# Optimization experiments

Hardware: AMD Instinct MI355X
Metric: run time of the kernel (lower is better)

The kernel has to match this reference:

```python
import jax, jax.numpy as jnp
import numpy as np

B, H, C_LEN, Q_LEN = 64, 128, 1024, 128


def setup_inputs() -> dict:
    key = jax.random.key(0)
    k1, k2, k3 = jax.random.split(key, 3)
    context = jax.random.normal(k1, (B, H, C_LEN), dtype=jnp.float32)
    question = jax.random.normal(k2, (B, H, Q_LEN), dtype=jnp.float32)
    lim = np.sqrt(1.0 / H)
    w = jax.random.uniform(k3, (3 * H,), dtype=jnp.float32, minval=-lim, maxval=lim)
    return {"context": context, "question": question, "w": w}


def reference(context, question, w):
    # context: (B, H, C), question: (B, H, Q); w: (3H,) with cat order (q, c, cq)
    h = w.shape[0] // 3
    w_q, w_c, w_cq = w[:h], w[h:2 * h], w[2 * h:]
    c = jnp.transpose(context, (0, 2, 1))   # (B, C, H)
    q = jnp.transpose(question, (0, 2, 1))  # (B, Q, H)
    # trilinear similarity s[b,i,j] = c_i.w_c + q_j.w_q + (c_i*w_cq).q_j  -> (B, C, Q)
    s = (c @ w_c)[:, :, None] + (q @ w_q)[:, None, :] \
        + jnp.einsum('bih,bjh->bij', c * w_cq, q)
    # original applies softmax over dim=1 (context axis) for BOTH s1 and s2
    s1 = jax.nn.softmax(s, axis=1)           # (B, C, Q)
    a = jnp.einsum('bij,bjh->bih', s1, q)    # (B, C, H)
    l = jnp.einsum('bij,bkj->bik', s1, s1)   # (B, C, C)
    b = jnp.einsum('bik,bkh->bih', l, c)     # (B, C, H)
    out = jnp.concatenate([c, a, c * a, c * b], axis=2)  # (B, C, 4H)
    # dropout disabled (drop_prob=0) for deterministic reference
    return jnp.transpose(out, (0, 2, 1))     # (B, 4H, C)
```

## Files before the change

### kernel.cpp

```cpp
#include <hip/hip_runtime.h>

#define BB 64
#define HH 128
#define CC 1024
#define QQ 128

typedef unsigned short u16;
typedef unsigned int u32;

__device__ __forceinline__ float lo2f(u32 u) {
  union { float f; u32 i; } v; v.i = u << 16; return v.f;
}
__device__ __forceinline__ float hi2f(u32 u) {
  union { float f; u32 i; } v; v.i = u & 0xFFFF0000u; return v.f;
}
__device__ __forceinline__ u16 f2b(float f) {
  union { float f; u32 i; } v; v.f = f;
  u32 r = v.i + 0x7FFFu + ((v.i >> 16) & 1u);
  return (u16)(r >> 16);
}

__global__ __launch_bounds__(512) void k1_s_softmax(
    const float* __restrict__ ctx, const float* __restrict__ qst,
    const float* __restrict__ w, u16* __restrict__ s1) {
  const int b = blockIdx.y;
  const int j0 = blockIdx.x * 16;
  const int tid = threadIdx.x;
  const float* cb = ctx + (size_t)b * HH * CC;
  const float* qb = qst + (size_t)b * HH * QQ;

  float dotv[16][2];
  float qwq[16];
  float cwc[2] = {0.f, 0.f};
#pragma unroll
  for (int jj = 0; jj < 16; ++jj) {
    qwq[jj] = 0.f;
    dotv[jj][0] = dotv[jj][1] = 0.f;
  }

  for (int h = 0; h < HH; ++h) {
    const float2 cv = *(const float2*)(cb + (size_t)h * CC + tid * 2);
    float c0 = cv.x, c1 = cv.y;
    float wqv = w[h], wcv = w[HH + h], wcqv = w[2 * HH + h];
    cwc[0] += c0 * wcv; cwc[1] += c1 * wcv;
    float t0 = c0 * wcqv, t1 = c1 * wcqv;
    const float4* qrow = (const float4*)(qb + (size_t)h * QQ + j0);
    float4 q0 = qrow[0], q1 = qrow[1], q2 = qrow[2], q3 = qrow[3];
    float qv[16] = {q0.x, q0.y, q0.z, q0.w, q1.x, q1.y, q1.z, q1.w,
                    q2.x, q2.y, q2.z, q2.w, q3.x, q3.y, q3.z, q3.w};
#pragma unroll
    for (int jj = 0; jj < 16; ++jj) {
      qwq[jj] += qv[jj] * wqv;
      dotv[jj][0] += t0 * qv[jj];
      dotv[jj][1] += t1 * qv[jj];
    }
  }
#pragma unroll
  for (int jj = 0; jj < 16; ++jj) {
    float base = qwq[jj];
    dotv[jj][0] += cwc[0] + base;
    dotv[jj][1] += cwc[1] + base;
  }

  __shared__ float red[16 * 512];
  __shared__ float red2[16 * 32];
  __shared__ float bc[16];
  const int rj = tid >> 5, rs = tid & 31;

#pragma unroll
  for (int jj = 0; jj < 16; ++jj)
    red[jj * 512 + tid] = fmaxf(dotv[jj][0], dotv[jj][1]);
  __syncthreads();
  {
    float m = red[rj * 512 + rs * 16];
#pragma unroll
    for (int g = 1; g < 16; ++g) m = fmaxf(m, red[rj * 512 + rs * 16 + g]);
    red2[rj * 32 + rs] = m;
  }
  __syncthreads();
  if (tid < 16) {
    float m = red2[tid * 32];
#pragma unroll
    for (int g = 1; g < 32; ++g) m = fmaxf(m, red2[tid * 32 + g]);
    bc[tid] = m;
  }
  __syncthreads();

#pragma unroll
  for (int jj = 0; jj < 16; ++jj) {
    float mj = bc[jj];
    float e0 = __expf(dotv[jj][0] - mj);
    float e1 = __expf(dotv[jj][1] - mj);
    dotv[jj][0] = e0; dotv[jj][1] = e1;
    red[jj * 512 + tid] = e0 + e1;
  }
  __syncthreads();
  {
    float s = 0.f;
#pragma unroll
    for (int g = 0; g < 16; ++g) s += red[rj * 512 + rs * 16 + g];
    red2[rj * 32 + rs] = s;
  }
  __syncthreads();
  if (tid < 16) {
    float s = 0.f;
#pragma unroll
    for (int g = 0; g < 32; ++g) s += red2[tid * 32 + g];
    bc[tid] = 1.0f / s;
  }
  __syncthreads();

  u16* srow = s1 + ((size_t)b * QQ + j0) * CC + tid * 2;
#pragma unroll
  for (int jj = 0; jj < 16; ++jj) {
    float inv = bc[jj];
    u32 pk = (u32)f2b(dotv[jj][0] * inv) | ((u32)f2b(dotv[jj][1] * inv) << 16);
    *(u32*)(srow + (size_t)jj * CC) = pk;
  }
}

__global__ __launch_bounds__(256) void k2_t(
    const float* __restrict__ ctx, const u16* __restrict__ s1,
    float* __restrict__ t) {
  const int b = blockIdx.y;
  const int tz = blockIdx.x;
  const int tile = tz & 3;
  const int z = tz >> 2;
  const int j0 = (tile & 1) * 64;
  const int h0 = (tile >> 1) * 64;
  const int tid = threadIdx.x;
  const int tj = tid >> 4, th = tid & 15;
  __shared__ float sA[64 * 33];
  __shared__ float sB[64 * 33];
  float acc[4][4];
#pragma unroll
  for (int jj = 0; jj < 4; ++jj)
#pragma unroll
    for (int hh = 0; hh < 4; ++hh) acc[jj][hh] = 0.f;

  const int r = tid >> 2;
  const int sg = (tid & 3) * 8;
  const u16* sbase = s1 + ((size_t)b * QQ + j0 + r) * CC + sg;
  const float* cbase = ctx + ((size_t)b * HH + h0 + r) * CC + sg;

  const int ib0 = z * 256;
  for (int ib = ib0; ib < ib0 + 256; ib += 32) {
    __syncthreads();
    {
      uint4 sv = *(const uint4*)(sbase + ib);
      float* a = &sA[r * 33 + sg];
      a[0] = lo2f(sv.x); a[1] = hi2f(sv.x);
      a[2] = lo2f(sv.y); a[3] = hi2f(sv.y);
      a[4] = lo2f(sv.z); a[5] = hi2f(sv.z);
      a[6] = lo2f(sv.w); a[7] = hi2f(sv.w);
      float4 c0 = *(const float4*)(cbase + ib);
      float4 c1 = *(const float4*)(cbase + ib + 4);
      float* bptr = &sB[r * 33 + sg];
      bptr[0] = c0.x; bptr[1] = c0.y; bptr[2] = c0.z; bptr[3] = c0.w;
      bptr[4] = c1.x; bptr[5] = c1.y; bptr[6] = c1.z; bptr[7] = c1.w;
    }
    __syncthreads();
#pragma unroll 4
    for (int ii = 0; ii < 32; ++ii) {
      float av[4], bv[4];
#pragma unroll
      for (int jj = 0; jj < 4; ++jj) av[jj] = sA[(tj + 16 * jj) * 33 + ii];
#pragma unroll
      for (int hh = 0; hh < 4; ++hh) bv[hh] = sB[(th + 16 * hh) * 33 + ii];
#pragma unroll
      for (int jj = 0; jj < 4; ++jj)
#pragma unroll
        for (int hh = 0; hh < 4; ++hh) acc[jj][hh] += av[jj] * bv[hh];
    }
  }
  float* tp = t + (size_t)b * QQ * HH;
#pragma unroll
  for (int jj = 0; jj < 4; ++jj)
#pragma unroll
    for (int hh = 0; hh < 4; ++hh)
      atomicAdd(&tp[(size_t)(j0 + tj + 16 * jj) * HH + (h0 + th + 16 * hh)],
                acc[jj][hh]);
}

__global__ __launch_bounds__(256) void k3_out(
    const float* __restrict__ ctx, const float* __restrict__ qst,
    const u16* __restrict__ s1, const float* __restrict__ t,
    float* __restrict__ out) {
  const int b = blockIdx.y;
  const int i0 = (blockIdx.x >> 1) * 64;
  const int h0 = (blockIdx.x & 1) * 64;
  const int tid = threadIdx.x;
  const int ti = tid & 15;
  const int th2 = tid >> 4;

  __shared__ float sA[32][65];
  __shared__ float sQ[32][65];
  __shared__ float sT[32][65];

  float accA[4][4], accB[4][4];
#pragma unroll
  for (int ii = 0; ii < 4; ++ii)
#pragma unroll
    for (int hh = 0; hh < 4; ++hh) { accA[ii][hh] = 0.f; accB[ii][hh] = 0.f; }

  for (int jc = 0; jc < QQ; jc += 32) {
    __syncthreads();
    {
      int rr = tid >> 3, col = (tid & 7) * 8;
      uint4 v = *(const uint4*)(s1 + ((size_t)b * QQ + jc + rr) * CC + i0 + col);
      float* dst = &sA[rr][col];
      dst[0] = lo2f(v.x); dst[1] = hi2f(v.x);
      dst[2] = lo2f(v.y); dst[3] = hi2f(v.y);
      dst[4] = lo2f(v.z); dst[5] = hi2f(v.z);
      dst[6] = lo2f(v.w); dst[7] = hi2f(v.w);
    }
    {
      int rr = tid >> 3, col = (tid & 7) * 8;
      const float* p = t + ((size_t)b * QQ + jc + rr) * HH + h0 + col;
      float4 v0 = *(const float4*)p;
      float4 v1 = *(const float4*)(p + 4);
      float* dst = &sT[rr][col];
      dst[0] = v0.x; dst[1] = v0.y; dst[2] = v0.z; dst[3] = v0.w;
      dst[4] = v1.x; dst[5] = v1.y; dst[6] = v1.z; dst[7] = v1.w;
    }
    {
      int hh = tid >> 2, jo = (tid & 3) * 8;
      const float* p = qst + ((size_t)b * HH + h0 + hh) * QQ + jc + jo;
      float4 v0 = *(const float4*)p;
      float4 v1 = *(const float4*)(p + 4);
      sQ[jo + 0][hh] = v0.x; sQ[jo + 1][hh] = v0.y;
      sQ[jo + 2][hh] = v0.z; sQ[jo + 3][hh] = v0.w;
      sQ[jo + 4][hh] = v1.x; sQ[jo + 5][hh] = v1.y;
      sQ[jo + 6][hh] = v1.z; sQ[jo + 7][hh] = v1.w;
    }
    __syncthreads();

#pragma unroll 8
    for (int kk = 0; kk < 32; ++kk) {
      float4 avv = *(const float4*)&sA[kk][ti * 4];
      float4 qvv = *(const float4*)&sQ[kk][th2 * 4];
      float4 tvv = *(const float4*)&sT[kk][th2 * 4];
      float av[4] = {avv.x, avv.y, avv.z, avv.w};
      float qv[4] = {qvv.x, qvv.y, qvv.z, qvv.w};
      float tv[4] = {tvv.x, tvv.y, tvv.z, tvv.w};
#pragma unroll
      for (int ii = 0; ii < 4; ++ii)
#pragma unroll
        for (int hh = 0; hh < 4; ++hh) {
          accA[ii][hh] += av[ii] * qv[hh];
          accB[ii][hh] += av[ii] * tv[hh];
        }
    }
  }

#pragma unroll
  for (int hh = 0; hh < 4; ++hh) {
    int h = h0 + th2 * 4 + hh;
    float4 cv = *(const float4*)(ctx + ((size_t)b * HH + h) * CC + i0 + ti * 4);
    float4 oA = {accA[0][hh], accA[1][hh], accA[2][hh], accA[3][hh]};
    float4 oB = {accB[0][hh], accB[1][hh], accB[2][hh], accB[3][hh]};
    float4 cA = {cv.x * oA.x, cv.y * oA.y, cv.z * oA.z, cv.w * oA.w};
    float4 cB = {cv.x * oB.x, cv.y * oB.y, cv.z * oB.z, cv.w * oB.w};
    size_t ob = (size_t)b * 4 * HH * CC + i0 + ti * 4;
    *(float4*)(out + ob + (size_t)h * CC) = cv;
    *(float4*)(out + ob + (size_t)(HH + h) * CC) = oA;
    *(float4*)(out + ob + (size_t)(2 * HH + h) * CC) = cA;
    *(float4*)(out + ob + (size_t)(3 * HH + h) * CC) = cB;
  }
}

extern "C" void kernel_launch(void* const* d_in, const int* in_sizes, int n_in,
                              void* d_out, int out_size, void* d_ws, size_t ws_size,
                              hipStream_t stream) {
  const float* ctx = (const float*)d_in[0];
  const float* qst = (const float*)d_in[1];
  const float* w = (const float*)d_in[2];
  for (int k = 0; k < n_in; ++k) {
    if (in_sizes[k] == BB * HH * CC) ctx = (const float*)d_in[k];
    else if (in_sizes[k] == BB * HH * QQ) qst = (const float*)d_in[k];
    else if (in_sizes[k] == 3 * HH) w = (const float*)d_in[k];
  }
  float* out = (float*)d_out;

  u16* s1 = (u16*)d_ws;
  float* t = (float*)((char*)d_ws + (size_t)BB * QQ * CC * sizeof(u16));

  k1_s_softmax<<<dim3(QQ / 16, BB), 512, 0, stream>>>(ctx, qst, w, s1);
  hipMemsetAsync(t, 0, (size_t)BB * QQ * HH * sizeof(float), stream);
  k2_t<<<dim3(16, BB), 256, 0, stream>>>(ctx, s1, t);
  k3_out<<<dim3(32, BB), 256, 0, stream>>>(ctx, qst, s1, t, out);
}
```

Before: 304.1 us.

## Port k2/k3 matmuls to bf16 MFMA with hi/lo split and transposed s1 layout

```diff
diff --git a/kernel.cpp b/kernel.cpp
--- a/kernel.cpp
+++ b/kernel.cpp
@@ -7,6 +7,10 @@
 
 typedef unsigned short u16;
 typedef unsigned int u32;
+using bf16x8 = __attribute__((ext_vector_type(8))) short;
+using f32x4 = __attribute__((ext_vector_type(4))) float;
+
+#define MFMA16(a, b, c) __builtin_amdgcn_mfma_f32_16x16x32_bf16(a, b, c, 0, 0, 0)
 
 __device__ __forceinline__ float lo2f(u32 u) {
   union { float f; u32 i; } v; v.i = u << 16; return v.f;
@@ -19,12 +23,41 @@
   u32 r = v.i + 0x7FFFu + ((v.i >> 16) & 1u);
   return (u16)(r >> 16);
 }
+__device__ __forceinline__ u32 pack_hi2(float a, float b) {
+  return (__float_as_uint(a) >> 16) | (__float_as_uint(b) & 0xFFFF0000u);
+}
+__device__ __forceinline__ u32 pack_lo2(float a, float b) {
+  float ra = a - __uint_as_float(__float_as_uint(a) & 0xFFFF0000u);
+  float rb = b - __uint_as_float(__float_as_uint(b) & 0xFFFF0000u);
+  return (__float_as_uint(ra) >> 16) | (__float_as_uint(rb) & 0xFFFF0000u);
+}
+
+__device__ __forceinline__ void stage16(const float* __restrict__ p,
+                                        u16* dhi, u16* dlo) {
+  float4 a0 = *(const float4*)p;
+  float4 a1 = *(const float4*)(p + 4);
+  float4 a2 = *(const float4*)(p + 8);
+  float4 a3 = *(const float4*)(p + 12);
+  uint4 h0 = {pack_hi2(a0.x, a0.y), pack_hi2(a0.z, a0.w),
+              pack_hi2(a1.x, a1.y), pack_hi2(a1.z, a1.w)};
+  uint4 h1 = {pack_hi2(a2.x, a2.y), pack_hi2(a2.z, a2.w),
+              pack_hi2(a3.x, a3.y), pack_hi2(a3.z, a3.w)};
+  uint4 l0 = {pack_lo2(a0.x, a0.y), pack_lo2(a0.z, a0.w),
+              pack_lo2(a1.x, a1.y), pack_lo2(a1.z, a1.w)};
+  uint4 l1 = {pack_lo2(a2.x, a2.y), pack_lo2(a2.z, a2.w),
+              pack_lo2(a3.x, a3.y), pack_lo2(a3.z, a3.w)};
+  *(uint4*)dhi = h0;
+  *(uint4*)(dhi + 8) = h1;
+  *(uint4*)dlo = l0;
+  *(uint4*)(dlo + 8) = l1;
+}
 
 __global__ __launch_bounds__(512) void k1_s_softmax(
     const float* __restrict__ ctx, const float* __restrict__ qst,
-    const float* __restrict__ w, u16* __restrict__ s1) {
-  const int b = blockIdx.y;
-  const int j0 = blockIdx.x * 16;
+    const float* __restrict__ w, u16* __restrict__ s1ws,
+    u16* __restrict__ s1tb) {
+  const int b = blockIdx.x;
+  const int j0 = blockIdx.y * 16;
   const int tid = threadIdx.x;
   const float* cb = ctx + (size_t)b * HH * CC;
   const float* qb = qst + (size_t)b * HH * QQ;
@@ -110,163 +143,181 @@
   }
   __syncthreads();
 
-  u16* srow = s1 + ((size_t)b * QQ + j0) * CC + tid * 2;
 #pragma unroll
   for (int jj = 0; jj < 16; ++jj) {
     float inv = bc[jj];
-    u32 pk = (u32)f2b(dotv[jj][0] * inv) | ((u32)f2b(dotv[jj][1] * inv) << 16);
+    dotv[jj][0] *= inv;
+    dotv[jj][1] *= inv;
+  }
+  u16* srow = s1ws + ((size_t)b * QQ + j0) * CC + tid * 2;
+#pragma unroll
+  for (int jj = 0; jj < 16; ++jj) {
+    u32 pk = (u32)f2b(dotv[jj][0]) | ((u32)f2b(dotv[jj][1]) << 16);
     *(u32*)(srow + (size_t)jj * CC) = pk;
   }
-}
-
-__global__ __launch_bounds__(256) void k2_t(
-    const float* __restrict__ ctx, const u16* __restrict__ s1,
-    float* __restrict__ t) {
-  const int b = blockIdx.y;
-  const int tz = blockIdx.x;
-  const int tile = tz & 3;
-  const int z = tz >> 2;
-  const int j0 = (tile & 1) * 64;
-  const int h0 = (tile >> 1) * 64;
+  u16* stb = s1tb + (size_t)b * (16 * 1024 * 8);
+  const int jg0 = j0 >> 3;
+#pragma unroll
+  for (int g = 0; g < 2; ++g) {
+#pragma unroll
+    for (int rr = 0; rr < 2; ++rr) {
+      const int o = g * 8;
+      uint4 v;
+      v.x = (u32)f2b(dotv[o + 0][rr]) | ((u32)f2b(dotv[o + 1][rr]) << 16);
+      v.y = (u32)f2b(dotv[o + 2][rr]) | ((u32)f2b(dotv[o + 3][rr]) << 16);
+      v.z = (u32)f2b(dotv[o + 4][rr]) | ((u32)f2b(dotv[o + 5][rr]) << 16);
+      v.w = (u32)f2b(dotv[o + 6][rr]) | ((u32)f2b(dotv[o + 7][rr]) << 16);
+      *(uint4*)(stb + ((size_t)(jg0 + g) * 1024 + (tid * 2 + rr)) * 8) = v;
+    }
+  }
+}
+
+__global__ __launch_bounds__(256, 2) void k2_t(
+    const float* __restrict__ ctx, const u16* __restrict__ s1ws,
+    float* __restrict__ tT) {
+  const int b = blockIdx.x;
+  const int kz = blockIdx.y;
   const int tid = threadIdx.x;
-  const int tj = tid >> 4, th = tid & 15;
-  __shared__ float sA[64 * 33];
-  __shared__ float sB[64 * 33];
-  float acc[4][4];
-#pragma unroll
-  for (int jj = 0; jj < 4; ++jj)
-#pragma unroll
-    for (int hh = 0; hh < 4; ++hh) acc[jj][hh] = 0.f;
-
-  const int r = tid >> 2;
-  const int sg = (tid & 3) * 8;
-  const u16* sbase = s1 + ((size_t)b * QQ + j0 + r) * CC + sg;
-  const float* cbase = ctx + ((size_t)b * HH + h0 + r) * CC + sg;
-
-  const int ib0 = z * 256;
-  for (int ib = ib0; ib < ib0 + 256; ib += 32) {
+  const int lane = tid & 63;
+  const int wv = tid >> 6;
+  const int l15 = lane & 15, l4 = lane >> 4;
+
+  __shared__ u16 sHi[128 * 32];
+  __shared__ u16 sLo[128 * 32];
+
+  f32x4 acc[2][8];
+#pragma unroll
+  for (int ht = 0; ht < 2; ++ht)
+#pragma unroll
+    for (int jt = 0; jt < 8; ++jt) acc[ht][jt] = 0.f;
+
+  const float* cb = ctx + (size_t)b * HH * CC;
+  const u16* sb = s1ws + (size_t)b * QQ * CC;
+  const int srow = tid >> 1;
+  const int scol = (tid & 1) * 16;
+
+  for (int ks = 0; ks < 4; ++ks) {
+    const int ib = kz * 128 + ks * 32;
     __syncthreads();
-    {
-      uint4 sv = *(const uint4*)(sbase + ib);
-      float* a = &sA[r * 33 + sg];
-      a[0] = lo2f(sv.x); a[1] = hi2f(sv.x);
-      a[2] = lo2f(sv.y); a[3] = hi2f(sv.y);
-      a[4] = lo2f(sv.z); a[5] = hi2f(sv.z);
-      a[6] = lo2f(sv.w); a[7] = hi2f(sv.w);
-      float4 c0 = *(const float4*)(cbase + ib);
-      float4 c1 = *(const float4*)(cbase + ib + 4);
-      float* bptr = &sB[r * 33 + sg];
-      bptr[0] = c0.x; bptr[1] = c0.y; bptr[2] = c0.z; bptr[3] = c0.w;
-      bptr[4] = c1.x; bptr[5] = c1.y; bptr[6] = c1.z; bptr[7] = c1.w;
-    }
+    stage16(cb + (size_t)srow * CC + ib + scol,
+            &sHi[srow * 32 + scol], &sLo[srow * 32 + scol]);
     __syncthreads();
-#pragma unroll 4
-    for (int ii = 0; ii < 32; ++ii) {
-      float av[4], bv[4];
-#pragma unroll
-      for (int jj = 0; jj < 4; ++jj) av[jj] = sA[(tj + 16 * jj) * 33 + ii];
-#pragma unroll
-      for (int hh = 0; hh < 4; ++hh) bv[hh] = sB[(th + 16 * hh) * 33 + ii];
-#pragma unroll
-      for (int jj = 0; jj < 4; ++jj)
-#pragma unroll
-        for (int hh = 0; hh < 4; ++hh) acc[jj][hh] += av[jj] * bv[hh];
-    }
-  }
-  float* tp = t + (size_t)b * QQ * HH;
-#pragma unroll
-  for (int jj = 0; jj < 4; ++jj)
-#pragma unroll
-    for (int hh = 0; hh < 4; ++hh)
-      atomicAdd(&tp[(size_t)(j0 + tj + 16 * jj) * HH + (h0 + th + 16 * hh)],
-                acc[jj][hh]);
-}
-
-__global__ __launch_bounds__(256) void k3_out(
+    bf16x8 aHi[2], aLo[2];
+#pragma unroll
+    for (int ht = 0; ht < 2; ++ht) {
+      const int ar = (wv * 32 + ht * 16 + l15) * 32 + l4 * 8;
+      aHi[ht] = *(const bf16x8*)&sHi[ar];
+      aLo[ht] = *(const bf16x8*)&sLo[ar];
+    }
+#pragma unroll
+    for (int jt = 0; jt < 8; ++jt) {
+      bf16x8 bf =
+          *(const bf16x8*)(sb + (size_t)(jt * 16 + l15) * CC + ib + l4 * 8);
+#pragma unroll
+      for (int ht = 0; ht < 2; ++ht) {
+        acc[ht][jt] = MFMA16(aHi[ht], bf, acc[ht][jt]);
+        acc[ht][jt] = MFMA16(aLo[ht], bf, acc[ht][jt]);
+      }
+    }
+  }
+  float* tb = tT + (size_t)b * HH * QQ;
+#pragma unroll
+  for (int ht = 0; ht < 2; ++ht)
+#pragma unroll
+    for (int jt = 0; jt < 8; ++jt)
+#pragma unroll
+      for (int r = 0; r < 4; ++r) {
+        const int h = wv * 32 + ht * 16 + l4 * 4 + r;
+        const int j = jt * 16 + l15;
+        atomicAdd(&tb[(size_t)h * QQ + j], acc[ht][jt][r]);
+      }
+}
+
+__global__ __launch_bounds__(256, 2) void k3_out(
     const float* __restrict__ ctx, const float* __restrict__ qst,
-    const u16* __restrict__ s1, const float* __restrict__ t,
+    const u16* __restrict__ s1tb, const float* __restrict__ tT,
     float* __restrict__ out) {
-  const int b = blockIdx.y;
-  const int i0 = (blockIdx.x >> 1) * 64;
-  const int h0 = (blockIdx.x & 1) * 64;
+  const int b = blockIdx.x;
+  const int i0 = blockIdx.y * 128;
   const int tid = threadIdx.x;
-  const int ti = tid & 15;
-  const int th2 = tid >> 4;
-
-  __shared__ float sA[32][65];
-  __shared__ float sQ[32][65];
-  __shared__ float sT[32][65];
-
-  float accA[4][4], accB[4][4];
-#pragma unroll
-  for (int ii = 0; ii < 4; ++ii)
-#pragma unroll
-    for (int hh = 0; hh < 4; ++hh) { accA[ii][hh] = 0.f; accB[ii][hh] = 0.f; }
-
-  for (int jc = 0; jc < QQ; jc += 32) {
+  const int lane = tid & 63;
+  const int wv = tid >> 6;
+  const int l15 = lane & 15, l4 = lane >> 4;
+
+  __shared__ u16 qHi[128 * 32], qLo[128 * 32];
+  __shared__ u16 tHi[128 * 32], tLo[128 * 32];
+
+  f32x4 accA[8][2], accB[8][2];
+#pragma unroll
+  for (int it = 0; it < 8; ++it)
+#pragma unroll
+    for (int ht = 0; ht < 2; ++ht) { accA[it][ht] = 0.f; accB[it][ht] = 0.f; }
+
+  const u16* stb = s1tb + (size_t)b * (16 * 1024 * 8);
+  const float* qb = qst + (size_t)b * HH * QQ;
+  const float* tb = tT + (size_t)b * HH * QQ;
+  const int srow = tid >> 1;
+  const int scol = (tid & 1) * 16;
+
+  for (int ks = 0; ks < 4; ++ks) {
+    const int jb = ks * 32;
     __syncthreads();
-    {
-      int rr = tid >> 3, col = (tid & 7) * 8;
-      uint4 v = *(const uint4*)(s1 + ((size_t)b * QQ + jc + rr) * CC + i0 + col);
-      float* dst = &sA[rr][col];
-      dst[0] = lo2f(v.x); dst[1] = hi2f(v.x);
-      dst[2] = lo2f(v.y); dst[3] = hi2f(v.y);
-      dst[4] = lo2f(v.z); dst[5] = hi2f(v.z);
-      dst[6] = lo2f(v.w); dst[7] = hi2f(v.w);
-    }
-    {
-      int rr = tid >> 3, col = (tid & 7) * 8;
-      const float* p = t + ((size_t)b * QQ + jc + rr) * HH + h0 + col;
-      float4 v0 = *(const float4*)p;
-      float4 v1 = *(const float4*)(p + 4);
-      float* dst = &sT[rr][col];
-      dst[0] = v0.x; dst[1] = v0.y; dst[2] = v0.z; dst[3] = v0.w;
-      dst[4] = v1.x; dst[5] = v1.y; dst[6] = v1.z; dst[7] = v1.w;
-    }
-    {
-      int hh = tid >> 2, jo = (tid & 3) * 8;
-      const float* p = qst + ((size_t)b * HH + h0 + hh) * QQ + jc + jo;
-      float4 v0 = *(const float4*)p;
-      float4 v1 = *(const float4*)(p + 4);
-      sQ[jo + 0][hh] = v0.x; sQ[jo + 1][hh] = v0.y;
-      sQ[jo + 2][hh] = v0.z; sQ[jo + 3][hh] = v0.w;
-      sQ[jo + 4][hh] = v1.x; sQ[jo + 5][hh] = v1.y;
-      sQ[jo + 6][hh] = v1.z; sQ[jo + 7][hh] = v1.w;
-    }
+    stage16(qb + (size_t)srow * QQ + jb + scol,
+            &qHi[srow * 32 + scol], &qLo[srow * 32 + scol]);
+    stage16(tb + (size_t)srow * QQ + jb + scol,
+            &tHi[srow * 32 + scol], &tLo[srow * 32 + scol]);
     __syncthreads();
-
-#pragma unroll 8
-    for (int kk = 0; kk < 32; ++kk) {
-      float4 avv = *(const float4*)&sA[kk][ti * 4];
-      float4 qvv = *(const float4*)&sQ[kk][th2 * 4];
-      float4 tvv = *(const float4*)&sT[kk][th2 * 4];
-      float av[4] = {avv.x, avv.y, avv.z, avv.w};
-      float qv[4] = {qvv.x, qvv.y, qvv.z, qvv.w};
-      float tv[4] = {tvv.x, tvv.y, tvv.z, tvv.w};
-#pragma unroll
-      for (int ii = 0; ii < 4; ++ii)
-#pragma unroll
-        for (int hh = 0; hh < 4; ++hh) {
-          accA[ii][hh] += av[ii] * qv[hh];
-          accB[ii][hh] += av[ii] * tv[hh];
+    bf16x8 qh[2], ql[2], th[2], tl[2];
+#pragma unroll
+    for (int ht = 0; ht < 2; ++ht) {
+      const int ar = (wv * 32 + ht * 16 + l15) * 32 + l4 * 8;
+      qh[ht] = *(const bf16x8*)&qHi[ar];
+      ql[ht] = *(const bf16x8*)&qLo[ar];
+      th[ht] = *(const bf16x8*)&tHi[ar];
+      tl[ht] = *(const bf16x8*)&tLo[ar];
+    }
+#pragma unroll
+    for (int half = 0; half < 2; ++half) {
+      bf16x8 af[4];
+#pragma unroll
+      for (int t4 = 0; t4 < 4; ++t4) {
+        const int it = half * 4 + t4;
+        af[t4] = *(const bf16x8*)(stb +
+            ((size_t)(ks * 4 + l4) * 1024 + i0 + it * 16 + l15) * 8);
+      }
+#pragma unroll
+      for (int t4 = 0; t4 < 4; ++t4) {
+        const int it = half * 4 + t4;
+#pragma unroll
+        for (int ht = 0; ht < 2; ++ht) {
+          accA[it][ht] = MFMA16(af[t4], qh[ht], accA[it][ht]);
+          accA[it][ht] = MFMA16(af[t4], ql[ht], accA[it][ht]);
+          accB[it][ht] = MFMA16(af[t4], th[ht], accB[it][ht]);
+          accB[it][ht] = MFMA16(af[t4], tl[ht], accB[it][ht]);
         }
-    }
-  }
-
-#pragma unroll
-  for (int hh = 0; hh < 4; ++hh) {
-    int h = h0 + th2 * 4 + hh;
-    float4 cv = *(const float4*)(ctx + ((size_t)b * HH + h) * CC + i0 + ti * 4);
-    float4 oA = {accA[0][hh], accA[1][hh], accA[2][hh], accA[3][hh]};
-    float4 oB = {accB[0][hh], accB[1][hh], accB[2][hh], accB[3][hh]};
-    float4 cA = {cv.x * oA.x, cv.y * oA.y, cv.z * oA.z, cv.w * oA.w};
-    float4 cB = {cv.x * oB.x, cv.y * oB.y, cv.z * oB.z, cv.w * oB.w};
-    size_t ob = (size_t)b * 4 * HH * CC + i0 + ti * 4;
-    *(float4*)(out + ob + (size_t)h * CC) = cv;
-    *(float4*)(out + ob + (size_t)(HH + h) * CC) = oA;
-    *(float4*)(out + ob + (size_t)(2 * HH + h) * CC) = cA;
-    *(float4*)(out + ob + (size_t)(3 * HH + h) * CC) = cB;
-  }
+      }
+    }
+  }
+
+  const float* cb = ctx + (size_t)b * HH * CC;
+  float* ob = out + (size_t)b * 4 * HH * CC;
+#pragma unroll
+  for (int it = 0; it < 8; ++it)
+#pragma unroll
+    for (int ht = 0; ht < 2; ++ht) {
+      const int h = wv * 32 + ht * 16 + l15;
+      const int ii = i0 + it * 16 + l4 * 4;
+      float4 cv = *(const float4*)(cb + (size_t)h * CC + ii);
+      f32x4 aA = accA[it][ht], aB = accB[it][ht];
+      float4 oA = {aA[0], aA[1], aA[2], aA[3]};
+      float4 cA = {cv.x * oA.x, cv.y * oA.y, cv.z * oA.z, cv.w * oA.w};
+      float4 cB = {cv.x * aB[0], cv.y * aB[1], cv.z * aB[2], cv.w * aB[3]};
+      const size_t base = (size_t)h * CC + ii;
+      *(float4*)(ob + base) = cv;
+      *(float4*)(ob + (size_t)HH * CC + base) = oA;
+      *(float4*)(ob + (size_t)2 * HH * CC + base) = cA;
+      *(float4*)(ob + (size_t)3 * HH * CC + base) = cB;
+    }
 }
 
 extern "C" void kernel_launch(void* const* d_in, const int* in_sizes, int n_in,
@@ -282,11 +333,12 @@
   }
   float* out = (float*)d_out;
 
-  u16* s1 = (u16*)d_ws;
-  float* t = (float*)((char*)d_ws + (size_t)BB * QQ * CC * sizeof(u16));
-
-  k1_s_softmax<<<dim3(QQ / 16, BB), 512, 0, stream>>>(ctx, qst, w, s1);
-  hipMemsetAsync(t, 0, (size_t)BB * QQ * HH * sizeof(float), stream);
-  k2_t<<<dim3(16, BB), 256, 0, stream>>>(ctx, s1, t);
-  k3_out<<<dim3(32, BB), 256, 0, stream>>>(ctx, qst, s1, t, out);
-}
+  u16* s1ws = (u16*)d_ws;
+  u16* s1tb = (u16*)((char*)d_ws + (size_t)16 * 1024 * 1024);
+  float* tT = (float*)((char*)d_ws + (size_t)32 * 1024 * 1024);
+
+  k1_s_softmax<<<dim3(BB, QQ / 16), 512, 0, stream>>>(ctx, qst, w, s1ws, s1tb);
+  hipMemsetAsync(tT, 0, (size_t)BB * QQ * HH * sizeof(float), stream);
+  k2_t<<<dim3(BB, 8), 256, 0, stream>>>(ctx, s1ws, tT);
+  k3_out<<<dim3(BB, 8), 256, 0, stream>>>(ctx, qst, s1tb, tT, out);
+}
```

New measurement: 271.8 us. 1.12x faster.
